# Optimization experiments

Hardware: AMD Instinct MI355X
Metric: run time of the kernel (lower is better)

Reference implementation:

```python
import jax, jax.numpy as jnp
import numpy as np

B, C, H, D, HID = 1024, 64, 64, 256, 256

def setup_inputs() -> dict:
    key = jax.random.key(0)
    k1, k2, k3, k4, k5, k6, k7, k8 = jax.random.split(key, 8)
    candidate_news_vector = jax.random.normal(k1, (B, C, D), dtype=jnp.float32)
    clicked_news_vector = jax.random.normal(k2, (B, H, D), dtype=jnp.float32)
    mask_cand = jax.random.randint(k3, (B, C), 0, 2).astype(bool).at[:, 0].set(True)
    mask_hist = jax.random.randint(k4, (B, H), 0, 2).astype(bool).at[:, 0].set(True)
    # nn.Linear default init: U(-1/sqrt(fan_in), 1/sqrt(fan_in))
    s1 = 1.0 / np.sqrt(2 * D)
    s2 = 1.0 / np.sqrt(HID)
    W1 = jax.random.uniform(k5, (HID, 2 * D), minval=-s1, maxval=s1, dtype=jnp.float32)
    b1 = jax.random.uniform(k6, (HID,), minval=-s1, maxval=s1, dtype=jnp.float32)
    W2 = jax.random.uniform(k7, (1, HID), minval=-s2, maxval=s2, dtype=jnp.float32)
    b2 = jax.random.uniform(k8, (1,), minval=-s2, maxval=s2, dtype=jnp.float32)
    return {"candidate_news_vector": candidate_news_vector,
            "clicked_news_vector": clicked_news_vector,
            "mask_cand": mask_cand, "mask_hist": mask_hist,
            "W1": W1, "b1": b1, "W2": W2, "b2": b2}

def reference(candidate_news_vector, clicked_news_vector, mask_cand, mask_hist, W1, b1, W2, b2):
    d = candidate_news_vector.shape[-1]
    w2 = W2[0]                                  # [HID]
    # Two stacked Linears with no nonlinearity collapse exactly:
    # score = (W2 @ W1_c) . cand + (W2 @ W1_h) . hist + (W2 @ b1 + b2)
    v_c = W1[:, :d].T @ w2                      # [D]
    v_h = W1[:, d:].T @ w2                      # [D]
    bias = jnp.dot(w2, b1) + b2[0]
    scores = (jnp.einsum('bcd,d->bc', candidate_news_vector, v_c)[:, :, None]
              + jnp.einsum('bhd,d->bh', clicked_news_vector, v_h)[:, None, :]
              + bias)                           # [B, C, H]
    neg = jnp.finfo(scores.dtype).min
    scores = jnp.where(mask_hist[:, None, :], scores, neg)
    weights = jax.nn.softmax(scores, axis=-1)   # [B, C, H]
    weights = jnp.where(mask_cand[:, :, None], weights, 0.0)
    user_vector = jnp.einsum('bch,bhd->bcd', weights, clicked_news_vector)
    return user_vector
```

## Files before the change

kernel.cpp:

```cpp
#include <hip/hip_runtime.h>
#include <math.h>

#define NB 1024
#define NC 64
#define NH 64
#define ND 256
#define NHID 256

typedef float f4 __attribute__((ext_vector_type(4)));

#define WS_PART_OFF 1024
#define WS_UV_OFF   32768

__device__ __forceinline__ bool read_mask(const void* m, int idx, int mode) {
  if (mode == 2) return ((const float*)m)[idx] != 0.0f;
  if (mode == 1) return ((const unsigned char*)m)[idx] != 0;
  return ((const int*)m)[idx] != 0;
}

__device__ __forceinline__ void detect_mode(const unsigned int* mask_cand,
                                            const unsigned int* mask_hist,
                                            int* dst) {
  int sawf = 0; unsigned int big = 0;
  for (int i = 0; i < 32; ++i) {
    unsigned int a = mask_hist[i], b = mask_cand[i];
    if (a == 0x3f800000u || b == 0x3f800000u) sawf = 1;
    if ((a > 1u && a != 0x3f800000u) || (b > 1u && b != 0x3f800000u)) big = 1;
  }
  *dst = sawf ? 2 : (big ? 1 : 0);
}

__global__ __launch_bounds__(256) void precompute_p1(
    const float* __restrict__ W1, const float* __restrict__ W2,
    float* __restrict__ ws)
{
  const int g = blockIdx.x;
  const int d = threadIdx.x;
  float acc = 0.f;
  #pragma unroll
  for (int jj = 0; jj < 4; ++jj) {
    int j = g * 4 + jj;
    acc = fmaf(W1[(size_t)j * (2 * ND) + ND + d], W2[j], acc);
  }
  ws[WS_PART_OFF + g * ND + d] = acc;
}

__global__ __launch_bounds__(256) void precompute_p2(
    const unsigned int* __restrict__ mask_cand,
    const unsigned int* __restrict__ mask_hist,
    float* __restrict__ ws)
{
  const int d = threadIdx.x;
  float acc = 0.f;
  #pragma unroll 8
  for (int g = 0; g < 64; ++g) acc += ws[WS_PART_OFF + g * ND + d];
  ws[d] = acc;
  if (d == 0) detect_mode(mask_cand, mask_hist, (int*)ws + ND);
}

__global__ __launch_bounds__(1024) void precompute_fallback(
    const float* __restrict__ W1, const float* __restrict__ W2,
    const unsigned int* __restrict__ mask_cand,
    const unsigned int* __restrict__ mask_hist,
    float* __restrict__ ws)
{
  __shared__ float w2_lds[NHID];
  __shared__ float partial[4][ND];
  int t = threadIdx.x;
  if (t < NHID) w2_lds[t] = W2[t];
  __syncthreads();
  int d = t & (ND - 1);
  int g = t >> 8;
  float acc = 0.f;
  #pragma unroll 8
  for (int j = g * 64; j < g * 64 + 64; ++j)
    acc = fmaf(W1[(size_t)j * (2 * ND) + ND + d], w2_lds[j], acc);
  partial[g][d] = acc;
  __syncthreads();
  if (t < ND)
    ws[t] = partial[0][t] + partial[1][t] + partial[2][t] + partial[3][t];
  if (t == 0) detect_mode(mask_cand, mask_hist, (int*)ws + ND);
}

template <int UV_STRIDE>
__global__ __launch_bounds__(512, 8) void score_uv_kernel(
    const float* __restrict__ hist,
    const void* __restrict__ mask_hist_v,
    const float* __restrict__ ws,
    float* __restrict__ uv_dst)
{
  const int b = blockIdx.x;
  const int t = threadIdx.x;
  const int lane = t & 63;
  const int g = t >> 6;

  __shared__ float s_lds[NH];
  __shared__ f4 part[8][64];

  const int mode = ((const int*)ws)[ND];
  const f4* hb4 = reinterpret_cast<const f4*>(hist + (size_t)b * NH * ND);
  const f4* vh4p = reinterpret_cast<const f4*>(ws);

  {
    const int r = t >> 3, cg = t & 7;
    float p = 0.f;
    #pragma unroll
    for (int i = 0; i < 8; ++i) {
      f4 x = hb4[r * 64 + i * 8 + cg];
      f4 v = vh4p[i * 8 + cg];
      p = fmaf(x.x, v.x, fmaf(x.y, v.y, fmaf(x.z, v.z, fmaf(x.w, v.w, p))));
    }
    p += __shfl_xor(p, 1); p += __shfl_xor(p, 2); p += __shfl_xor(p, 4);
    if (cg == 0)
      s_lds[r] = read_mask(mask_hist_v, b * NH + r, mode) ? p : -3.0e38f;
  }
  __syncthreads();

  float wval;
  {
    float s = s_lds[lane];
    float m = s;
    #pragma unroll
    for (int off = 32; off; off >>= 1) m = fmaxf(m, __shfl_xor(m, off));
    float e = expf(s - m);
    float sum = e;
    #pragma unroll
    for (int off = 32; off; off >>= 1) sum += __shfl_xor(sum, off);
    wval = e / sum;
  }

  {
    f4 acc = {0.f, 0.f, 0.f, 0.f};
    #pragma unroll
    for (int j = 0; j < 8; ++j) {
      float wj = __shfl(wval, g * 8 + j);
      f4 x = hb4[(g * 8 + j) * 64 + lane];
      acc += wj * x;
    }
    part[g][lane] = acc;
  }
  __syncthreads();

  if (t < 64) {
    f4 uv = part[0][t];
    #pragma unroll
    for (int q = 1; q < 8; ++q) uv += part[q][t];
    reinterpret_cast<f4*>(uv_dst + (size_t)b * UV_STRIDE)[t] = uv;
  }
}

__global__ __launch_bounds__(256) void broadcast_kernel(
    const float* __restrict__ uv_src,
    const void* __restrict__ mask_cand_v,
    const float* __restrict__ ws,
    float* __restrict__ out)
{
  const int bid = blockIdx.x;
  const int b = bid >> 2, q = bid & 3;
  const int t = threadIdx.x, lane = t & 63, g = t >> 6;
  const int mode = ((const int*)ws)[ND];
  const f4 uv = reinterpret_cast<const f4*>(uv_src + (size_t)b * ND)[lane];
  f4* ob4 = reinterpret_cast<f4*>(out + (size_t)b * NC * ND);
  const f4 zero = {0.f, 0.f, 0.f, 0.f};
  #pragma unroll
  for (int j = 0; j < 4; ++j) {
    int c = q * 16 + g * 4 + j;
    bool mc = read_mask(mask_cand_v, b * NC + c, mode);
    f4 val = mc ? uv : zero;
    __builtin_nontemporal_store(val, &ob4[c * 64 + lane]);
  }
}

__global__ __launch_bounds__(256) void broadcast_stash_kernel(
    const void* __restrict__ mask_cand_v,
    const float* __restrict__ ws,
    float* __restrict__ out)
{
  const int b = blockIdx.x;
  const int t = threadIdx.x, lane = t & 63, g = t >> 6;
  const int mode = ((const int*)ws)[ND];
  f4* ob4 = reinterpret_cast<f4*>(out + (size_t)b * NC * ND);
  const f4 uv = reinterpret_cast<const f4*>(ob4)[lane];
  __syncthreads();
  const f4 zero = {0.f, 0.f, 0.f, 0.f};
  #pragma unroll
  for (int k = 0; k < 16; ++k) {
    int c = g * 16 + k;
    bool mc = read_mask(mask_cand_v, b * NC + c, mode);
    f4 val = mc ? uv : zero;
    __builtin_nontemporal_store(val, &ob4[c * 64 + lane]);
  }
}

extern "C" void kernel_launch(void* const* d_in, const int* in_sizes, int n_in,
                              void* d_out, int out_size, void* d_ws, size_t ws_size,
                              hipStream_t stream) {
  (void)in_sizes; (void)n_in; (void)out_size;
  const float* hist = (const float*)d_in[1];
  const void*  mask_cand = d_in[2];
  const void*  mask_hist = d_in[3];
  const float* W1 = (const float*)d_in[4];
  const float* W2 = (const float*)d_in[6];
  float* ws = (float*)d_ws;
  float* out = (float*)d_out;

  const bool mid = ws_size >= (size_t)(WS_PART_OFF + 64 * ND) * sizeof(float);
  const bool big = ws_size >= (size_t)(WS_UV_OFF + NB * ND) * sizeof(float);

  if (mid) {
    precompute_p1<<<64, 256, 0, stream>>>(W1, W2, ws);
    precompute_p2<<<1, 256, 0, stream>>>(
        (const unsigned int*)mask_cand, (const unsigned int*)mask_hist, ws);
  } else {
    precompute_fallback<<<1, 1024, 0, stream>>>(
        W1, W2, (const unsigned int*)mask_cand, (const unsigned int*)mask_hist, ws);
  }

  if (big) {
    score_uv_kernel<ND><<<NB, 512, 0, stream>>>(hist, mask_hist, ws, ws + WS_UV_OFF);
    broadcast_kernel<<<NB * 4, 256, 0, stream>>>(ws + WS_UV_OFF, mask_cand, ws, out);
  } else {
    score_uv_kernel<NC * ND><<<NB, 512, 0, stream>>>(hist, mask_hist, ws, out);
    broadcast_stash_kernel<<<NB, 256, 0, stream>>>(mask_cand, ws, out);
  }
}
```

Baseline: 47.76 us.

## Split score pass into streaming kernel and fuse weighted-sum with broadcast

The stage boundary moves. One streaming kernel computes the history scores, one wave per 8 rows, and writes them to workspace. A second kernel per batch then applies masking and softmax, does the weighted sum over history, and writes the masked broadcast output straight away, so the separate user-vector round trip and broadcast kernel go away. The history tensor is now read twice, once per kernel, and the result depends on that second read hitting cache. The small-workspace fallback also fuses the broadcast into its single kernel.

Result: slower. 50.21 us (+5.1%).

```diff
diff --git a/kernel.cpp b/kernel.cpp
--- a/kernel.cpp
+++ b/kernel.cpp
@@ -10,7 +10,7 @@
 typedef float f4 __attribute__((ext_vector_type(4)));
 
 #define WS_PART_OFF 1024
-#define WS_UV_OFF   32768
+#define WS_S_OFF    32768
 
 __device__ __forceinline__ bool read_mask(const void* m, int idx, int mode) {
   if (mode == 2) return ((const float*)m)[idx] != 0.0f;
@@ -30,6 +30,13 @@
   *dst = sawf ? 2 : (big ? 1 : 0);
 }
 
+__device__ __forceinline__ float dot4(f4 a, f4 b) {
+  return fmaf(a.x, b.x, fmaf(a.y, b.y, fmaf(a.z, b.z, a.w * b.w)));
+}
+
+#define BFLY(p) { p += __shfl_xor(p, 32); p += __shfl_xor(p, 16); p += __shfl_xor(p, 8); \
+                  p += __shfl_xor(p, 4);  p += __shfl_xor(p, 2);  p += __shfl_xor(p, 1); }
+
 __global__ __launch_bounds__(256) void precompute_p1(
     const float* __restrict__ W1, const float* __restrict__ W2,
     float* __restrict__ ws)
@@ -82,23 +89,99 @@
   if (t == 0) detect_mode(mask_cand, mask_hist, (int*)ws + ND);
 }
 
-template <int UV_STRIDE>
-__global__ __launch_bounds__(512, 8) void score_uv_kernel(
+__global__ __launch_bounds__(256) void score_stream_kernel(
     const float* __restrict__ hist,
+    const float* __restrict__ ws,
+    float* __restrict__ s_out)
+{
+  const int t = threadIdx.x, lane = t & 63;
+  const int W = blockIdx.x * 4 + (t >> 6);
+  const f4* h4 = reinterpret_cast<const f4*>(hist) + (size_t)W * 512;
+  const f4 vh = reinterpret_cast<const f4*>(ws)[lane];
+
+  f4 x0 = h4[0 * 64 + lane], x1 = h4[1 * 64 + lane];
+  f4 x2 = h4[2 * 64 + lane], x3 = h4[3 * 64 + lane];
+  f4 x4 = h4[4 * 64 + lane], x5 = h4[5 * 64 + lane];
+  f4 x6 = h4[6 * 64 + lane], x7 = h4[7 * 64 + lane];
+
+  float p0 = dot4(x0, vh), p1 = dot4(x1, vh), p2 = dot4(x2, vh), p3 = dot4(x3, vh);
+  float p4 = dot4(x4, vh), p5 = dot4(x5, vh), p6 = dot4(x6, vh), p7 = dot4(x7, vh);
+  BFLY(p0) BFLY(p1) BFLY(p2) BFLY(p3) BFLY(p4) BFLY(p5) BFLY(p6) BFLY(p7)
+
+  float v = p0;
+  if (lane == 1) v = p1;  if (lane == 2) v = p2;  if (lane == 3) v = p3;
+  if (lane == 4) v = p4;  if (lane == 5) v = p5;  if (lane == 6) v = p6;
+  if (lane == 7) v = p7;
+  if (lane < 8) s_out[W * 8 + lane] = v;
+}
+
+__global__ __launch_bounds__(256) void uv_bcast_kernel(
+    const float* __restrict__ hist,
+    const void* __restrict__ mask_cand_v,
     const void* __restrict__ mask_hist_v,
     const float* __restrict__ ws,
-    float* __restrict__ uv_dst)
+    const float* __restrict__ s_in,
+    float* __restrict__ out)
+{
+  const int b = blockIdx.x, t = threadIdx.x, lane = t & 63, w = t >> 6;
+  __shared__ float w_lds[NH];
+  __shared__ f4 red[4][64];
+
+  const int mode = ((const int*)ws)[ND];
+  const f4* hb4 = reinterpret_cast<const f4*>(hist) + (size_t)b * 4096;
+
+  f4 xr[16];
+  #pragma unroll
+  for (int k = 0; k < 16; ++k) xr[k] = hb4[k * 256 + t];
+
+  if (t < 64) {
+    float s = read_mask(mask_hist_v, b * NH + t, mode) ? s_in[b * NH + t] : -3.0e38f;
+    float m = s;
+    m = fmaxf(m, __shfl_xor(m, 32)); m = fmaxf(m, __shfl_xor(m, 16));
+    m = fmaxf(m, __shfl_xor(m, 8));  m = fmaxf(m, __shfl_xor(m, 4));
+    m = fmaxf(m, __shfl_xor(m, 2));  m = fmaxf(m, __shfl_xor(m, 1));
+    float e = expf(s - m);
+    float sum = e;
+    BFLY(sum)
+    w_lds[t] = e / sum;
+  }
+  __syncthreads();
+
+  f4 acc = {0.f, 0.f, 0.f, 0.f};
+  #pragma unroll
+  for (int k = 0; k < 16; ++k) acc += w_lds[k * 4 + w] * xr[k];
+  red[w][lane] = acc;
+  __syncthreads();
+
+  f4 uv = red[0][lane] + red[1][lane] + red[2][lane] + red[3][lane];
+  f4* ob4 = reinterpret_cast<f4*>(out) + (size_t)b * 4096;
+  const f4 zero = {0.f, 0.f, 0.f, 0.f};
+  #pragma unroll
+  for (int k = 0; k < 16; ++k) {
+    int c = k * 4 + w;
+    bool mc = read_mask(mask_cand_v, b * NC + c, mode);
+    f4 val = mc ? uv : zero;
+    __builtin_nontemporal_store(val, &ob4[k * 256 + t]);
+  }
+}
+
+__global__ __launch_bounds__(512, 8) void fused_fallback_kernel(
+    const float* __restrict__ hist,
+    const void* __restrict__ mask_cand_v,
+    const void* __restrict__ mask_hist_v,
+    const float* __restrict__ ws,
+    float* __restrict__ out)
 {
   const int b = blockIdx.x;
   const int t = threadIdx.x;
   const int lane = t & 63;
-  const int g = t >> 6;
+  const int w = t >> 6;
 
   __shared__ float s_lds[NH];
   __shared__ f4 part[8][64];
 
   const int mode = ((const int*)ws)[ND];
-  const f4* hb4 = reinterpret_cast<const f4*>(hist + (size_t)b * NH * ND);
+  const f4* hb4 = reinterpret_cast<const f4*>(hist) + (size_t)b * 4096;
   const f4* vh4p = reinterpret_cast<const f4*>(ws);
 
   {
@@ -133,62 +216,27 @@
     f4 acc = {0.f, 0.f, 0.f, 0.f};
     #pragma unroll
     for (int j = 0; j < 8; ++j) {
-      float wj = __shfl(wval, g * 8 + j);
-      f4 x = hb4[(g * 8 + j) * 64 + lane];
+      float wj = __shfl(wval, w * 8 + j);
+      f4 x = hb4[(w * 8 + j) * 64 + lane];
       acc += wj * x;
     }
-    part[g][lane] = acc;
-  }
-  __syncthreads();
-
-  if (t < 64) {
-    f4 uv = part[0][t];
-    #pragma unroll
-    for (int q = 1; q < 8; ++q) uv += part[q][t];
-    reinterpret_cast<f4*>(uv_dst + (size_t)b * UV_STRIDE)[t] = uv;
-  }
-}
-
-__global__ __launch_bounds__(256) void broadcast_kernel(
-    const float* __restrict__ uv_src,
-    const void* __restrict__ mask_cand_v,
-    const float* __restrict__ ws,
-    float* __restrict__ out)
-{
-  const int bid = blockIdx.x;
-  const int b = bid >> 2, q = bid & 3;
-  const int t = threadIdx.x, lane = t & 63, g = t >> 6;
-  const int mode = ((const int*)ws)[ND];
-  const f4 uv = reinterpret_cast<const f4*>(uv_src + (size_t)b * ND)[lane];
-  f4* ob4 = reinterpret_cast<f4*>(out + (size_t)b * NC * ND);
-  const f4 zero = {0.f, 0.f, 0.f, 0.f};
-  #pragma unroll
-  for (int j = 0; j < 4; ++j) {
-    int c = q * 16 + g * 4 + j;
-    bool mc = read_mask(mask_cand_v, b * NC + c, mode);
-    f4 val = mc ? uv : zero;
-    __builtin_nontemporal_store(val, &ob4[c * 64 + lane]);
-  }
-}
-
-__global__ __launch_bounds__(256) void broadcast_stash_kernel(
-    const void* __restrict__ mask_cand_v,
-    const float* __restrict__ ws,
-    float* __restrict__ out)
-{
-  const int b = blockIdx.x;
-  const int t = threadIdx.x, lane = t & 63, g = t >> 6;
-  const int mode = ((const int*)ws)[ND];
-  f4* ob4 = reinterpret_cast<f4*>(out + (size_t)b * NC * ND);
-  const f4 uv = reinterpret_cast<const f4*>(ob4)[lane];
-  __syncthreads();
-  const f4 zero = {0.f, 0.f, 0.f, 0.f};
-  #pragma unroll
-  for (int k = 0; k < 16; ++k) {
-    int c = g * 16 + k;
-    bool mc = read_mask(mask_cand_v, b * NC + c, mode);
-    f4 val = mc ? uv : zero;
-    __builtin_nontemporal_store(val, &ob4[c * 64 + lane]);
+    part[w][lane] = acc;
+  }
+  __syncthreads();
+
+  {
+    f4 uv = part[0][lane];
+    #pragma unroll
+    for (int g = 1; g < 8; ++g) uv += part[g][lane];
+    f4* ob4 = reinterpret_cast<f4*>(out) + (size_t)b * 4096;
+    const f4 zero = {0.f, 0.f, 0.f, 0.f};
+    #pragma unroll
+    for (int k = 0; k < 8; ++k) {
+      int c = w + k * 8;
+      bool mc = read_mask(mask_cand_v, b * NC + c, mode);
+      f4 val = mc ? uv : zero;
+      __builtin_nontemporal_store(val, &ob4[c * 64 + lane]);
+    }
   }
 }
 
@@ -205,7 +253,7 @@
   float* out = (float*)d_out;
 
   const bool mid = ws_size >= (size_t)(WS_PART_OFF + 64 * ND) * sizeof(float);
-  const bool big = ws_size >= (size_t)(WS_UV_OFF + NB * ND) * sizeof(float);
+  const bool big = ws_size >= (size_t)(WS_S_OFF + NB * NH) * sizeof(float);
 
   if (mid) {
     precompute_p1<<<64, 256, 0, stream>>>(W1, W2, ws);
@@ -217,10 +265,10 @@
   }
 
   if (big) {
-    score_uv_kernel<ND><<<NB, 512, 0, stream>>>(hist, mask_hist, ws, ws + WS_UV_OFF);
-    broadcast_kernel<<<NB * 4, 256, 0, stream>>>(ws + WS_UV_OFF, mask_cand, ws, out);
+    score_stream_kernel<<<2048, 256, 0, stream>>>(hist, ws, ws + WS_S_OFF);
+    uv_bcast_kernel<<<NB, 256, 0, stream>>>(hist, mask_cand, mask_hist, ws,
+                                            ws + WS_S_OFF, out);
   } else {
-    score_uv_kernel<NC * ND><<<NB, 512, 0, stream>>>(hist, mask_hist, ws, out);
-    broadcast_stash_kernel<<<NB, 256, 0, stream>>>(mask_cand, ws, out);
-  }
-}
+    fused_fallback_kernel<<<NB, 512, 0, stream>>>(hist, mask_cand, mask_hist, ws, out);
+  }
+}
```
